# Performance work log

Hardware: AMD Instinct MI355X
Metric: run time of the kernel (lower is better)

Reference implementation:

```python
import jax, jax.numpy as jnp
import numpy as np

B, T, C = 2, 4096, 512
H, DH = 8, 64            # num_heads, num_head_channels (per-head dim after reshape)
COND = 512
SCALE = (DH // H) ** -0.5  # faithful to original: (num_head_channels // num_heads)**-0.5


def setup_inputs() -> dict:
    key = jax.random.key(0)
    ks = jax.random.split(key, 6)
    x = jax.random.normal(ks[0], (B, T, C), dtype=jnp.float32)
    condition = jax.random.normal(ks[1], (B, T, COND), dtype=jnp.float32)
    W_qk = jax.random.normal(ks[2], (COND, 2 * H * DH), dtype=jnp.float32) * (COND ** -0.5)
    W_v = jax.random.normal(ks[3], (C, H * DH), dtype=jnp.float32) * (C ** -0.5)
    W_u = jax.random.normal(ks[4], (H * DH, C), dtype=jnp.float32) * ((H * DH) ** -0.5)
    b_u = jax.random.normal(ks[5], (C,), dtype=jnp.float32) * 0.01
    return {"x": x, "condition": condition, "W_qk": W_qk, "W_v": W_v, "W_u": W_u, "b_u": b_u}


def reference(x, condition, W_qk, W_v, W_u, b_u):
    b, t, _ = x.shape
    qk = condition @ W_qk                                  # [b, t, 2*H*DH]
    q, k = jnp.split(qk, 2, axis=-1)
    q = q.reshape(b, t, H, DH).transpose(0, 2, 1, 3)       # [b, H, t, DH]
    k = k.reshape(b, t, H, DH).transpose(0, 2, 1, 3)
    v = (x @ W_v).reshape(b, t, H, DH).transpose(0, 2, 1, 3)
    q = q * SCALE
    dots = jnp.einsum('bhid,bhjd->bhij', q, k)             # [b, H, t, t] (1 GB score matrix)
    attn = jax.nn.softmax(dots, axis=-1)
    out = jnp.einsum('bhij,bhjd->bhid', attn, v)           # [b, H, t, DH]
    out = out.transpose(0, 2, 1, 3).reshape(b, t, H * DH)
    return out @ W_u + b_u
```

## Files before the change

kernel.cpp:

```cpp
#include <hip/hip_runtime.h>

#define B_SZ 2
#define T_SZ 4096

typedef unsigned short u16;
typedef __attribute__((ext_vector_type(8))) short short8;
typedef __attribute__((ext_vector_type(4))) float f32x4;
typedef __attribute__((ext_vector_type(4))) unsigned short u16x4;

#define CEXP 0.51006973f

__device__ __forceinline__ u16 f2bf(float f) {
    unsigned int u;
    __builtin_memcpy(&u, &f, 4);
    u = (u + 0x7fffu + ((u >> 16) & 1u)) >> 16;
    return (u16)u;
}
__device__ __forceinline__ unsigned int rbits(float f) {
    unsigned int u;
    __builtin_memcpy(&u, &f, 4);
    return u + 0x8000u;
}
__device__ __forceinline__ f32x4 mfma16(short8 a, short8 b, f32x4 c) {
    return __builtin_amdgcn_mfma_f32_16x16x32_bf16(a, b, c, 0, 0, 0);
}

__global__ void k_prep(const float* __restrict__ Wqk, const float* __restrict__ Wv,
                       const float* __restrict__ Wu, u16* __restrict__ Wqk_t,
                       u16* __restrict__ Wv_t, u16* __restrict__ Wu_t) {
    int blk = blockIdx.x, tid = threadIdx.x;
    __shared__ u16 T[64][72];
    const float* src; u16* dst; int N, ti;
    if (blk < 128)      { src = Wqk; dst = Wqk_t; N = 1024; ti = blk; }
    else if (blk < 192) { src = Wv;  dst = Wv_t;  N = 512;  ti = blk - 128; }
    else                { src = Wu;  dst = Wu_t;  N = 512;  ti = blk - 192; }
    int nt = N >> 6;
    int bi = ti / nt, bj = ti - bi * nt;
    int kb = bi * 64, nb = bj * 64;
    int r = tid >> 2, c4 = (tid & 3) * 16;
#pragma unroll
    for (int jj = 0; jj < 4; ++jj) {
        float4 v = *(const float4*)(src + (size_t)(kb + r) * N + nb + c4 + jj * 4);
        u16x4 w = { f2bf(v.x), f2bf(v.y), f2bf(v.z), f2bf(v.w) };
        *(u16x4*)(&T[r][c4 + jj * 4]) = w;
    }
    __syncthreads();
#pragma unroll
    for (int jj = 0; jj < 4; ++jj) {
        int c = c4 + jj * 4;
        u16x4 w = { T[c][r], T[c + 1][r], T[c + 2][r], T[c + 3][r] };
        *(u16x4*)(dst + (size_t)(nb + r) * 512 + kb + c) = w;
    }
}

template <typename OutT, int MODE, bool AF32, bool BF32, int TM, int TN>
__device__ __forceinline__ void gemm_body(int m0, int n0,
                                          const void* __restrict__ Ap, const void* __restrict__ Bp,
                                          const float* __restrict__ bias, OutT* __restrict__ C,
                                          OutT* __restrict__ C2, u16* As, u16* Bs) {
    const int K = 512;
    constexpr int BK = 64;
    constexpr int MI = TM / 32, NJ = TN / 32;
    constexpr int NAF = TM / 16, NAB = TM / 32;
    constexpr int NBF = TN / 16, NBB = TN / 32;
    int tid = threadIdx.x;
    int wave = tid >> 6, lane = tid & 63, l16 = lane & 15, q = lane >> 4;
    int mo = (wave & 1) * (TM / 2), no = (wave >> 1) * (TN / 2);

    f32x4 acc[MI][NJ];
#pragma unroll
    for (int i = 0; i < MI; ++i)
#pragma unroll
        for (int j = 0; j < NJ; ++j) acc[i][j] = (f32x4){0.f, 0.f, 0.f, 0.f};

    const float* Af = (const float*)Ap; const u16* Ab = (const u16*)Ap;
    const float* Bf = (const float*)Bp; const u16* Bb = (const u16*)Bp;

    const float* apf[NAF > 0 ? NAF : 1]; const u16* apb[NAB > 0 ? NAB : 1];
    const float* bpf[NBF > 0 ? NBF : 1]; const u16* bpb[NBB > 0 ? NBB : 1];
    float4 raf[NAF > 0 ? NAF : 1], rbf[NBF > 0 ? NBF : 1];
    short8 rab[NAB > 0 ? NAB : 1], rbb[NBB > 0 ? NBB : 1];

    if constexpr (AF32) {
#pragma unroll
        for (int jj = 0; jj < NAF; ++jj) {
            int id = tid + 256 * jj;
            apf[jj] = Af + (size_t)(m0 + (id >> 4)) * K + (id & 15) * 4;
            raf[jj] = *(const float4*)(apf[jj]);
        }
    } else {
#pragma unroll
        for (int jj = 0; jj < NAB; ++jj) {
            int id = tid + 256 * jj;
            apb[jj] = Ab + (size_t)(m0 + (id >> 3)) * K + (id & 7) * 8;
            rab[jj] = *(const short8*)(apb[jj]);
        }
    }
    if constexpr (BF32) {
#pragma unroll
        for (int jj = 0; jj < NBF; ++jj) {
            int id = tid + 256 * jj;
            bpf[jj] = Bf + (size_t)(n0 + (id >> 4)) * K + (id & 15) * 4;
            rbf[jj] = *(const float4*)(bpf[jj]);
        }
    } else {
#pragma unroll
        for (int jj = 0; jj < NBB; ++jj) {
            int id = tid + 256 * jj;
            bpb[jj] = Bb + (size_t)(n0 + (id >> 3)) * K + (id & 7) * 8;
            rbb[jj] = *(const short8*)(bpb[jj]);
        }
    }

#pragma unroll 1
    for (int k0 = 0; k0 < K; k0 += BK) {
        __syncthreads();
        if constexpr (AF32) {
#pragma unroll
            for (int jj = 0; jj < NAF; ++jj) {
                int id = tid + 256 * jj;
                u16x4 w = { f2bf(raf[jj].x), f2bf(raf[jj].y), f2bf(raf[jj].z), f2bf(raf[jj].w) };
                *(u16x4*)(&As[(id >> 4) * 72 + (id & 15) * 4]) = w;
            }
        } else {
#pragma unroll
            for (int jj = 0; jj < NAB; ++jj) {
                int id = tid + 256 * jj;
                *(short8*)(&As[(id >> 3) * 72 + (id & 7) * 8]) = rab[jj];
            }
        }
        if constexpr (BF32) {
#pragma unroll
            for (int jj = 0; jj < NBF; ++jj) {
                int id = tid + 256 * jj;
                u16x4 w = { f2bf(rbf[jj].x), f2bf(rbf[jj].y), f2bf(rbf[jj].z), f2bf(rbf[jj].w) };
                *(u16x4*)(&Bs[(id >> 4) * 72 + (id & 15) * 4]) = w;
            }
        } else {
#pragma unroll
            for (int jj = 0; jj < NBB; ++jj) {
                int id = tid + 256 * jj;
                *(short8*)(&Bs[(id >> 3) * 72 + (id & 7) * 8]) = rbb[jj];
            }
        }
        __syncthreads();

        int kadv = (k0 + BK < K) ? BK : 0;
        if constexpr (AF32) {
#pragma unroll
            for (int jj = 0; jj < NAF; ++jj) { apf[jj] += kadv; raf[jj] = *(const float4*)(apf[jj]); }
        } else {
#pragma unroll
            for (int jj = 0; jj < NAB; ++jj) { apb[jj] += kadv; rab[jj] = *(const short8*)(apb[jj]); }
        }
        if constexpr (BF32) {
#pragma unroll
            for (int jj = 0; jj < NBF; ++jj) { bpf[jj] += kadv; rbf[jj] = *(const float4*)(bpf[jj]); }
        } else {
#pragma unroll
            for (int jj = 0; jj < NBB; ++jj) { bpb[jj] += kadv; rbb[jj] = *(const short8*)(bpb[jj]); }
        }
        __builtin_amdgcn_sched_barrier(0);

#pragma unroll
        for (int kk = 0; kk < 2; ++kk) {
            short8 af[MI], bf[NJ];
#pragma unroll
            for (int i = 0; i < MI; ++i)
                af[i] = *(const short8*)(&As[(mo + i * 16 + l16) * 72 + kk * 32 + q * 8]);
#pragma unroll
            for (int j = 0; j < NJ; ++j)
                bf[j] = *(const short8*)(&Bs[(no + j * 16 + l16) * 72 + kk * 32 + q * 8]);
#pragma unroll
            for (int i = 0; i < MI; ++i)
#pragma unroll
                for (int j = 0; j < NJ; ++j) acc[i][j] = mfma16(af[i], bf[j], acc[i][j]);
        }
    }

#pragma unroll
    for (int i = 0; i < MI; ++i) {
        int mb = m0 + mo + i * 16 + q * 4;
#pragma unroll
        for (int j = 0; j < NJ; ++j) {
            int nc = n0 + no + j * 16 + l16;
            if constexpr (MODE == 0) {
                float4 bb = *(const float4*)(bias + mb);
                float4 w = { acc[i][j][0] + bb.x, acc[i][j][1] + bb.y,
                             acc[i][j][2] + bb.z, acc[i][j][3] + bb.w };
                *(float4*)(&C[(size_t)nc * 512 + mb]) = w;
            } else if constexpr (MODE == 1) {
                int b = nc >> 12, t = nc & 4095;
                int h = (mb & 511) >> 6, d = mb & 63;
                size_t addr = ((size_t)((b * 8 + h) * 4096 + t)) * 64 + d;
                if (mb < 512) {
                    u16x4 w = { f2bf(acc[i][j][0] * CEXP), f2bf(acc[i][j][1] * CEXP),
                                f2bf(acc[i][j][2] * CEXP), f2bf(acc[i][j][3] * CEXP) };
                    *(u16x4*)(&C[addr]) = w;
                } else {
                    u16x4 w = { f2bf(acc[i][j][0]), f2bf(acc[i][j][1]),
                                f2bf(acc[i][j][2]), f2bf(acc[i][j][3]) };
                    *(u16x4*)(&C2[addr]) = w;
                }
            } else {
                int b = mb >> 12, t = mb & 4095;
                int kt = t >> 6, k64 = t & 63;
                int h = nc >> 6, d = nc & 63;
                size_t addr = ((((size_t)(b * 8 + h) * 64 + kt) * 64 + d) << 6) + k64;
                u16x4 w = { f2bf(acc[i][j][0]), f2bf(acc[i][j][1]),
                            f2bf(acc[i][j][2]), f2bf(acc[i][j][3]) };
                *(u16x4*)(&C[addr]) = w;
            }
        }
    }
}

__global__ __launch_bounds__(256) void k_qkv(const u16* __restrict__ Wqk_t, const float* __restrict__ cond,
                                             const float* __restrict__ x, const u16* __restrict__ Wv_t,
                                             u16* __restrict__ Qh, u16* __restrict__ Kh,
                                             u16* __restrict__ Vb) {
    __shared__ __align__(16) u16 smem[(128 + 128) * 72];
    u16* As = smem;
    u16* Bs = smem + 128 * 72;
    int bid = blockIdx.x;
    if (bid < 512) {
        int bx = bid >> 6, by = bid & 63;
        gemm_body<u16, 1, false, true, 128, 128>(bx * 128, by * 128, Wqk_t, cond, nullptr, Qh, Kh, As, Bs);
    } else {
        int bid2 = bid - 512;
        int by = bid2 >> 6, bx = bid2 & 63;
        gemm_body<u16, 2, true, false, 128, 128>(bx * 128, by * 128, x, Wv_t, nullptr, Vb, nullptr, As, Bs);
    }
}

__global__ __launch_bounds__(256) void k_out(const u16* __restrict__ Wu_t, const u16* __restrict__ at,
                                             const float* __restrict__ bu, float* __restrict__ out) {
    __shared__ __align__(16) u16 smem[(128 + 128) * 72];
    int bid = blockIdx.x;
    int bx = bid >> 6, by = bid & 63;
    gemm_body<float, 0, false, false, 128, 128>(bx * 128, by * 128, Wu_t, at, bu, out, nullptr,
                                                smem, smem + 128 * 72);
}

__global__ __launch_bounds__(512) void k_flash(const u16* __restrict__ Qh, const u16* __restrict__ Kh,
                                               const u16* __restrict__ Vb, u16* __restrict__ o) {
    int bid = blockIdx.x;
    int h = bid & 7, qt = (bid >> 3) & 31, b = bid >> 8;
    int tid = threadIdx.x;
    int wave = tid >> 6, lane = tid & 63, l16 = lane & 15, q = lane >> 4;
    int ks = wave >> 2, w4 = wave & 3;
    int t256 = tid & 255;

    __shared__ __align__(16) u16 smem[2 * (64 * 80 + 64 * 72)];
    u16* Kt = smem + ks * (64 * 80 + 64 * 72);
    u16* Vt = Kt + 64 * 80;

    int head = b * 8 + h;
    short8 qf[2][2];
#pragma unroll
    for (int g = 0; g < 2; ++g) {
        const u16* qp = Qh + ((size_t)head * 4096 + qt * 128 + g * 64 + w4 * 16 + l16) * 64 + q * 8;
        qf[g][0] = *(const short8*)(qp);
        qf[g][1] = *(const short8*)(qp + 32);
    }

    const u16* kb = Kh + (size_t)head * 4096 * 64;
    const u16* vb = Vb + (size_t)head * 4096 * 64;

    int r0 = t256 >> 3, g0 = t256 & 7;
    u16* kw0 = &Kt[r0 * 80 + g0 * 8];
    u16* kw1 = &Kt[(r0 + 32) * 80 + g0 * 8];
    u16* vw0 = &Vt[r0 * 72 + g0 * 8];
    u16* vw1 = &Vt[(r0 + 32) * 72 + g0 * 8];

    f32x4 oacc[2][4];
#pragma unroll
    for (int g = 0; g < 2; ++g)
#pragma unroll
        for (int c = 0; c < 4; ++c) oacc[g][c] = (f32x4){0.f, 0.f, 0.f, 0.f};
    f32x4 lacc[2];
    lacc[0] = (f32x4){0.f, 0.f, 0.f, 0.f};
    lacc[1] = (f32x4){0.f, 0.f, 0.f, 0.f};
    const short8 ones = { 0x3F80, 0x3F80, 0x3F80, 0x3F80, 0x3F80, 0x3F80, 0x3F80, 0x3F80 };
    int pi0 = (l16 >> 2) * 8 + (l16 & 3);

    size_t off0 = (size_t)(ks * 32 + (qt & 31)) * 4096;
    short8 rk0 = *(const short8*)(kb + off0 + t256 * 8);
    short8 rk1 = *(const short8*)(kb + off0 + t256 * 8 + 2048);
    short8 rv0 = *(const short8*)(vb + off0 + t256 * 8);
    short8 rv1 = *(const short8*)(vb + off0 + t256 * 8 + 2048);

#pragma unroll 1
    for (int it = 0; it < 32; ++it) {
        __syncthreads();
        *(short8*)kw0 = rk0;
        *(short8*)kw1 = rk1;
        *(short8*)vw0 = rv0;
        *(short8*)vw1 = rv1;
        __syncthreads();

        size_t offn = (size_t)(ks * 32 + ((qt + it + 1) & 31)) * 4096;
        rk0 = *(const short8*)(kb + offn + t256 * 8);
        rk1 = *(const short8*)(kb + offn + t256 * 8 + 2048);
        rv0 = *(const short8*)(vb + offn + t256 * 8);
        rv1 = *(const short8*)(vb + offn + t256 * 8 + 2048);
        __builtin_amdgcn_sched_barrier(0);

#pragma unroll
        for (int kk = 0; kk < 2; ++kk) {
            const u16* ka = &Kt[(kk * 32 + pi0) * 80 + q * 8];
            short8 A00 = *(const short8*)(ka);
            short8 A01 = *(const short8*)(ka + 32);
            short8 A10 = *(const short8*)(ka + 4 * 80);
            short8 A11 = *(const short8*)(ka + 4 * 80 + 32);
            short8 vfc[4];
#pragma unroll
            for (int c = 0; c < 4; ++c)
                vfc[c] = *(const short8*)(&Vt[(c * 16 + l16) * 72 + kk * 32 + q * 8]);

#pragma unroll
            for (int g = 0; g < 2; ++g) {
                f32x4 s0 = (f32x4){0.f, 0.f, 0.f, 0.f};
                f32x4 s1 = (f32x4){0.f, 0.f, 0.f, 0.f};
                s0 = mfma16(A00, qf[g][0], s0); s0 = mfma16(A01, qf[g][1], s0);
                s1 = mfma16(A10, qf[g][0], s1); s1 = mfma16(A11, qf[g][1], s1);

                uint4 pd;
                pd.x = __builtin_amdgcn_perm(rbits(__builtin_amdgcn_exp2f(s0[1])),
                                             rbits(__builtin_amdgcn_exp2f(s0[0])), 0x07060302u);
                pd.y = __builtin_amdgcn_perm(rbits(__builtin_amdgcn_exp2f(s0[3])),
                                             rbits(__builtin_amdgcn_exp2f(s0[2])), 0x07060302u);
                pd.z = __builtin_amdgcn_perm(rbits(__builtin_amdgcn_exp2f(s1[1])),
                                             rbits(__builtin_amdgcn_exp2f(s1[0])), 0x07060302u);
                pd.w = __builtin_amdgcn_perm(rbits(__builtin_amdgcn_exp2f(s1[3])),
                                             rbits(__builtin_amdgcn_exp2f(s1[2])), 0x07060302u);
                short8 pf;
                __builtin_memcpy(&pf, &pd, 16);

                lacc[g] = mfma16(ones, pf, lacc[g]);
#pragma unroll
                for (int c = 0; c < 4; ++c)
                    oacc[g][c] = mfma16(vfc[c], pf, oacc[g][c]);
            }
        }
    }

    __syncthreads();
    float* red = (float*)smem;
    if (ks == 1) {
        float* rp = red + ((w4 * 64 + lane) * 37);
#pragma unroll
        for (int g = 0; g < 2; ++g)
#pragma unroll
            for (int c = 0; c < 4; ++c)
#pragma unroll
                for (int r = 0; r < 4; ++r) rp[g * 16 + c * 4 + r] = oacc[g][c][r];
        rp[32] = lacc[0][0];
        rp[33] = lacc[1][0];
    }
    __syncthreads();
    if (ks == 0) {
        const float* rp = red + ((w4 * 64 + lane) * 37);
#pragma unroll
        for (int g = 0; g < 2; ++g) {
#pragma unroll
            for (int c = 0; c < 4; ++c)
#pragma unroll
                for (int r = 0; r < 4; ++r) oacc[g][c][r] += rp[g * 16 + c * 4 + r];
            float inv = 1.f / (lacc[g][0] + rp[32 + g]);
            u16* ob = o + (size_t)(b * T_SZ + qt * 128 + g * 64 + w4 * 16 + l16) * 512 + h * 64 + q * 4;
#pragma unroll
            for (int c = 0; c < 4; ++c) {
                u16x4 w = { f2bf(oacc[g][c][0] * inv), f2bf(oacc[g][c][1] * inv),
                            f2bf(oacc[g][c][2] * inv), f2bf(oacc[g][c][3] * inv) };
                *(u16x4*)(ob + c * 16) = w;
            }
        }
    }
}

extern "C" void kernel_launch(void* const* d_in, const int* in_sizes, int n_in,
                              void* d_out, int out_size, void* d_ws, size_t ws_size,
                              hipStream_t stream) {
    const float* x    = (const float*)d_in[0];
    const float* cond = (const float*)d_in[1];
    const float* Wqk  = (const float*)d_in[2];
    const float* Wv   = (const float*)d_in[3];
    const float* Wu   = (const float*)d_in[4];
    const float* bu   = (const float*)d_in[5];
    float* out = (float*)d_out;

    const size_t MT = (size_t)B_SZ * T_SZ;
    u16* qh_ws = (u16*)d_ws;
    u16* kh_ws = qh_ws + MT * 512;
    u16* vb_ws = kh_ws + MT * 512;
    u16* at_ws = vb_ws + MT * 512;
    u16* Wqk_t = at_ws + MT * 512;
    u16* Wv_t  = Wqk_t + (size_t)1024 * 512;
    u16* Wu_t  = Wv_t + (size_t)512 * 512;

    k_prep<<<256, 256, 0, stream>>>(Wqk, Wv, Wu, Wqk_t, Wv_t, Wu_t);
    k_qkv<<<768, 256, 0, stream>>>(Wqk_t, cond, x, Wv_t, qh_ws, kh_ws, vb_ws);
    k_flash<<<512, 512, 0, stream>>>(qh_ws, kh_ws, vb_ws, at_ws);
    k_out<<<256, 256, 0, stream>>>(Wu_t, at_ws, bu, out);
}
```

Baseline: 203.3 us.

## Double-buffer flash K/V tiles and use direct global-to-LDS loads for bf16 GEMM weights

```diff
diff --git a/kernel.cpp b/kernel.cpp
--- a/kernel.cpp
+++ b/kernel.cpp
@@ -23,6 +23,10 @@
 }
 __device__ __forceinline__ f32x4 mfma16(short8 a, short8 b, f32x4 c) {
     return __builtin_amdgcn_mfma_f32_16x16x32_bf16(a, b, c, 0, 0, 0);
+}
+__device__ __forceinline__ void glds16(const u16* g, u16* l) {
+    __builtin_amdgcn_global_load_lds((const __attribute__((address_space(1))) void*)g,
+                                     (__attribute__((address_space(3))) void*)l, 16, 0, 0);
 }
 
 __global__ void k_prep(const float* __restrict__ Wqk, const float* __restrict__ Wv,
@@ -49,11 +53,14 @@
     for (int jj = 0; jj < 4; ++jj) {
         int c = c4 + jj * 4;
         u16x4 w = { T[c][r], T[c + 1][r], T[c + 2][r], T[c + 3][r] };
-        *(u16x4*)(dst + (size_t)(nb + r) * 512 + kb + c) = w;
-    }
-}
-
-template <typename OutT, int MODE, bool AF32, bool BF32, int TM, int TN>
+        int csw = (c & 7) | ((((c >> 3) ^ (r & 7))) << 3);
+        *(u16x4*)(dst + (size_t)(nb + r) * 512 + kb + csw) = w;
+    }
+}
+
+enum { ST_GLDS = 0, ST_F32 = 1, ST_BF16 = 2 };
+
+template <typename OutT, int MODE, int SA, int SB, int TM, int TN>
 __device__ __forceinline__ void gemm_body(int m0, int n0,
                                           const void* __restrict__ Ap, const void* __restrict__ Bp,
                                           const float* __restrict__ bias, OutT* __restrict__ C,
@@ -61,8 +68,8 @@
     const int K = 512;
     constexpr int BK = 64;
     constexpr int MI = TM / 32, NJ = TN / 32;
-    constexpr int NAF = TM / 16, NAB = TM / 32;
-    constexpr int NBF = TN / 16, NBB = TN / 32;
+    constexpr int NAF = TM / 16, NAB = TM / 32, NAG = TM / 32;
+    constexpr int NBF = TN / 16, NBB = TN / 32, NBG = TN / 32;
     int tid = threadIdx.x;
     int wave = tid >> 6, lane = tid & 63, l16 = lane & 15, q = lane >> 4;
     int mo = (wave & 1) * (TM / 2), no = (wave >> 1) * (TN / 2);
@@ -81,14 +88,14 @@
     float4 raf[NAF > 0 ? NAF : 1], rbf[NBF > 0 ? NBF : 1];
     short8 rab[NAB > 0 ? NAB : 1], rbb[NBB > 0 ? NBB : 1];
 
-    if constexpr (AF32) {
+    if constexpr (SA == ST_F32) {
 #pragma unroll
         for (int jj = 0; jj < NAF; ++jj) {
             int id = tid + 256 * jj;
             apf[jj] = Af + (size_t)(m0 + (id >> 4)) * K + (id & 15) * 4;
             raf[jj] = *(const float4*)(apf[jj]);
         }
-    } else {
+    } else if constexpr (SA == ST_BF16) {
 #pragma unroll
         for (int jj = 0; jj < NAB; ++jj) {
             int id = tid + 256 * jj;
@@ -96,14 +103,14 @@
             rab[jj] = *(const short8*)(apb[jj]);
         }
     }
-    if constexpr (BF32) {
+    if constexpr (SB == ST_F32) {
 #pragma unroll
         for (int jj = 0; jj < NBF; ++jj) {
             int id = tid + 256 * jj;
             bpf[jj] = Bf + (size_t)(n0 + (id >> 4)) * K + (id & 15) * 4;
             rbf[jj] = *(const float4*)(bpf[jj]);
         }
-    } else {
+    } else if constexpr (SB == ST_BF16) {
 #pragma unroll
         for (int jj = 0; jj < NBB; ++jj) {
             int id = tid + 256 * jj;
@@ -115,48 +122,64 @@
 #pragma unroll 1
     for (int k0 = 0; k0 < K; k0 += BK) {
         __syncthreads();
-        if constexpr (AF32) {
+        if constexpr (SA == ST_F32) {
 #pragma unroll
             for (int jj = 0; jj < NAF; ++jj) {
                 int id = tid + 256 * jj;
                 u16x4 w = { f2bf(raf[jj].x), f2bf(raf[jj].y), f2bf(raf[jj].z), f2bf(raf[jj].w) };
                 *(u16x4*)(&As[(id >> 4) * 72 + (id & 15) * 4]) = w;
             }
-        } else {
+        } else if constexpr (SA == ST_BF16) {
 #pragma unroll
             for (int jj = 0; jj < NAB; ++jj) {
                 int id = tid + 256 * jj;
                 *(short8*)(&As[(id >> 3) * 72 + (id & 7) * 8]) = rab[jj];
             }
         }
-        if constexpr (BF32) {
+        if constexpr (SB == ST_F32) {
 #pragma unroll
             for (int jj = 0; jj < NBF; ++jj) {
                 int id = tid + 256 * jj;
                 u16x4 w = { f2bf(rbf[jj].x), f2bf(rbf[jj].y), f2bf(rbf[jj].z), f2bf(rbf[jj].w) };
                 *(u16x4*)(&Bs[(id >> 4) * 72 + (id & 15) * 4]) = w;
             }
-        } else {
+        } else if constexpr (SB == ST_BF16) {
 #pragma unroll
             for (int jj = 0; jj < NBB; ++jj) {
                 int id = tid + 256 * jj;
                 *(short8*)(&Bs[(id >> 3) * 72 + (id & 7) * 8]) = rbb[jj];
             }
         }
+        if constexpr (SA == ST_GLDS) {
+            const u16* gbase = Ab + (size_t)m0 * K + k0;
+#pragma unroll
+            for (int jj = 0; jj < NAG; ++jj) {
+                int e = jj * 2048 + tid * 8;
+                glds16(gbase + (size_t)(e >> 6) * K + (e & 63), &As[e]);
+            }
+        }
+        if constexpr (SB == ST_GLDS) {
+            const u16* gbase = Bb + (size_t)n0 * K + k0;
+#pragma unroll
+            for (int jj = 0; jj < NBG; ++jj) {
+                int e = jj * 2048 + tid * 8;
+                glds16(gbase + (size_t)(e >> 6) * K + (e & 63), &Bs[e]);
+            }
+        }
         __syncthreads();
 
         int kadv = (k0 + BK < K) ? BK : 0;
-        if constexpr (AF32) {
+        if constexpr (SA == ST_F32) {
 #pragma unroll
             for (int jj = 0; jj < NAF; ++jj) { apf[jj] += kadv; raf[jj] = *(const float4*)(apf[jj]); }
-        } else {
+        } else if constexpr (SA == ST_BF16) {
 #pragma unroll
             for (int jj = 0; jj < NAB; ++jj) { apb[jj] += kadv; rab[jj] = *(const short8*)(apb[jj]); }
         }
-        if constexpr (BF32) {
+        if constexpr (SB == ST_F32) {
 #pragma unroll
             for (int jj = 0; jj < NBF; ++jj) { bpf[jj] += kadv; rbf[jj] = *(const float4*)(bpf[jj]); }
-        } else {
+        } else if constexpr (SB == ST_BF16) {
 #pragma unroll
             for (int jj = 0; jj < NBB; ++jj) { bpb[jj] += kadv; rbb[jj] = *(const short8*)(bpb[jj]); }
         }
@@ -166,11 +189,21 @@
         for (int kk = 0; kk < 2; ++kk) {
             short8 af[MI], bf[NJ];
 #pragma unroll
-            for (int i = 0; i < MI; ++i)
-                af[i] = *(const short8*)(&As[(mo + i * 16 + l16) * 72 + kk * 32 + q * 8]);
-#pragma unroll
-            for (int j = 0; j < NJ; ++j)
-                bf[j] = *(const short8*)(&Bs[(no + j * 16 + l16) * 72 + kk * 32 + q * 8]);
+            for (int i = 0; i < MI; ++i) {
+                int r = mo + i * 16 + l16;
+                if constexpr (SA == ST_GLDS)
+                    af[i] = *(const short8*)(&As[r * 64 + (((kk * 4 + q) ^ (l16 & 7)) << 3)]);
+                else
+                    af[i] = *(const short8*)(&As[r * 72 + kk * 32 + q * 8]);
+            }
+#pragma unroll
+            for (int j = 0; j < NJ; ++j) {
+                int r = no + j * 16 + l16;
+                if constexpr (SB == ST_GLDS)
+                    bf[j] = *(const short8*)(&Bs[r * 64 + (((kk * 4 + q) ^ (l16 & 7)) << 3)]);
+                else
+                    bf[j] = *(const short8*)(&Bs[r * 72 + kk * 32 + q * 8]);
+            }
 #pragma unroll
             for (int i = 0; i < MI; ++i)
 #pragma unroll
@@ -219,27 +252,27 @@
                                              const float* __restrict__ x, const u16* __restrict__ Wv_t,
                                              u16* __restrict__ Qh, u16* __restrict__ Kh,
                                              u16* __restrict__ Vb) {
-    __shared__ __align__(16) u16 smem[(128 + 128) * 72];
-    u16* As = smem;
-    u16* Bs = smem + 128 * 72;
+    __shared__ __align__(16) u16 smem[128 * 64 + 128 * 72];
     int bid = blockIdx.x;
     if (bid < 512) {
         int bx = bid >> 6, by = bid & 63;
-        gemm_body<u16, 1, false, true, 128, 128>(bx * 128, by * 128, Wqk_t, cond, nullptr, Qh, Kh, As, Bs);
+        gemm_body<u16, 1, ST_GLDS, ST_F32, 128, 128>(bx * 128, by * 128, Wqk_t, cond, nullptr,
+                                                     Qh, Kh, smem, smem + 128 * 64);
     } else {
         int bid2 = bid - 512;
         int by = bid2 >> 6, bx = bid2 & 63;
-        gemm_body<u16, 2, true, false, 128, 128>(bx * 128, by * 128, x, Wv_t, nullptr, Vb, nullptr, As, Bs);
+        gemm_body<u16, 2, ST_F32, ST_GLDS, 128, 128>(bx * 128, by * 128, x, Wv_t, nullptr,
+                                                     Vb, nullptr, smem, smem + 128 * 72);
     }
 }
 
 __global__ __launch_bounds__(256) void k_out(const u16* __restrict__ Wu_t, const u16* __restrict__ at,
                                              const float* __restrict__ bu, float* __restrict__ out) {
-    __shared__ __align__(16) u16 smem[(128 + 128) * 72];
+    __shared__ __align__(16) u16 smem[128 * 64 + 128 * 72];
     int bid = blockIdx.x;
     int bx = bid >> 6, by = bid & 63;
-    gemm_body<float, 0, false, false, 128, 128>(bx * 128, by * 128, Wu_t, at, bu, out, nullptr,
-                                                smem, smem + 128 * 72);
+    gemm_body<float, 0, ST_GLDS, ST_BF16, 128, 128>(bx * 128, by * 128, Wu_t, at, bu, out, nullptr,
+                                                    smem, smem + 128 * 64);
 }
 
 __global__ __launch_bounds__(512) void k_flash(const u16* __restrict__ Qh, const u16* __restrict__ Kh,
@@ -251,9 +284,10 @@
     int ks = wave >> 2, w4 = wave & 3;
     int t256 = tid & 255;
 
-    __shared__ __align__(16) u16 smem[2 * (64 * 80 + 64 * 72)];
-    u16* Kt = smem + ks * (64 * 80 + 64 * 72);
-    u16* Vt = Kt + 64 * 80;
+    const int TSZ = 64 * 80 + 64 * 72;
+    __shared__ __align__(16) u16 smem[2 * 2 * (64 * 80 + 64 * 72)];
+    u16* Kt0 = smem + ks * 2 * TSZ;
+    u16* Vt0 = Kt0 + 64 * 80;
 
     int head = b * 8 + h;
     short8 qf[2][2];
@@ -268,10 +302,10 @@
     const u16* vb = Vb + (size_t)head * 4096 * 64;
 
     int r0 = t256 >> 3, g0 = t256 & 7;
-    u16* kw0 = &Kt[r0 * 80 + g0 * 8];
-    u16* kw1 = &Kt[(r0 + 32) * 80 + g0 * 8];
-    u16* vw0 = &Vt[r0 * 72 + g0 * 8];
-    u16* vw1 = &Vt[(r0 + 32) * 72 + g0 * 8];
+    u16* kw0 = &Kt0[r0 * 80 + g0 * 8];
+    u16* kw1 = &Kt0[(r0 + 32) * 80 + g0 * 8];
+    u16* vw0 = &Vt0[r0 * 72 + g0 * 8];
+    u16* vw1 = &Vt0[(r0 + 32) * 72 + g0 * 8];
 
     f32x4 oacc[2][4];
 #pragma unroll
@@ -284,31 +318,43 @@
     const short8 ones = { 0x3F80, 0x3F80, 0x3F80, 0x3F80, 0x3F80, 0x3F80, 0x3F80, 0x3F80 };
     int pi0 = (l16 >> 2) * 8 + (l16 & 3);
 
-    size_t off0 = (size_t)(ks * 32 + (qt & 31)) * 4096;
-    short8 rk0 = *(const short8*)(kb + off0 + t256 * 8);
-    short8 rk1 = *(const short8*)(kb + off0 + t256 * 8 + 2048);
-    short8 rv0 = *(const short8*)(vb + off0 + t256 * 8);
-    short8 rv1 = *(const short8*)(vb + off0 + t256 * 8 + 2048);
+    size_t offA = (size_t)(ks * 32 + (qt & 31)) * 4096;
+    short8 rk0 = *(const short8*)(kb + offA + t256 * 8);
+    short8 rk1 = *(const short8*)(kb + offA + t256 * 8 + 2048);
+    short8 rv0 = *(const short8*)(vb + offA + t256 * 8);
+    short8 rv1 = *(const short8*)(vb + offA + t256 * 8 + 2048);
+    *(short8*)kw0 = rk0;
+    *(short8*)kw1 = rk1;
+    *(short8*)vw0 = rv0;
+    *(short8*)vw1 = rv1;
+    size_t offB = (size_t)(ks * 32 + ((qt + 1) & 31)) * 4096;
+    rk0 = *(const short8*)(kb + offB + t256 * 8);
+    rk1 = *(const short8*)(kb + offB + t256 * 8 + 2048);
+    rv0 = *(const short8*)(vb + offB + t256 * 8);
+    rv1 = *(const short8*)(vb + offB + t256 * 8 + 2048);
 
 #pragma unroll 1
     for (int it = 0; it < 32; ++it) {
         __syncthreads();
-        *(short8*)kw0 = rk0;
-        *(short8*)kw1 = rk1;
-        *(short8*)vw0 = rv0;
-        *(short8*)vw1 = rv1;
-        __syncthreads();
-
-        size_t offn = (size_t)(ks * 32 + ((qt + it + 1) & 31)) * 4096;
+        int wb = (it + 1) & 1;
+        *(short8*)(kw0 + wb * TSZ) = rk0;
+        *(short8*)(kw1 + wb * TSZ) = rk1;
+        *(short8*)(vw0 + wb * TSZ) = rv0;
+        *(short8*)(vw1 + wb * TSZ) = rv1;
+
+        size_t offn = (size_t)(ks * 32 + ((qt + it + 2) & 31)) * 4096;
         rk0 = *(const short8*)(kb + offn + t256 * 8);
         rk1 = *(const short8*)(kb + offn + t256 * 8 + 2048);
         rv0 = *(const short8*)(vb + offn + t256 * 8);
         rv1 = *(const short8*)(vb + offn + t256 * 8 + 2048);
         __builtin_amdgcn_sched_barrier(0);
 
+        const u16* Ktc = Kt0 + (it & 1) * TSZ;
+        const u16* Vtc = Ktc + 64 * 80;
+
 #pragma unroll
         for (int kk = 0; kk < 2; ++kk) {
-            const u16* ka = &Kt[(kk * 32 + pi0) * 80 + q * 8];
+            const u16* ka = &Ktc[(kk * 32 + pi0) * 80 + q * 8];
             short8 A00 = *(const short8*)(ka);
             short8 A01 = *(const short8*)(ka + 32);
             short8 A10 = *(const short8*)(ka + 4 * 80);
@@ -316,7 +362,7 @@
             short8 vfc[4];
 #pragma unroll
             for (int c = 0; c < 4; ++c)
-                vfc[c] = *(const short8*)(&Vt[(c * 16 + l16) * 72 + kk * 32 + q * 8]);
+                vfc[c] = *(const short8*)(&Vtc[(c * 16 + l16) * 72 + kk * 32 + q * 8]);
 
 #pragma unroll
             for (int g = 0; g < 2; ++g) {
```

Result: slower. 208.0 us (+2.3%).

## Use direct global-to-LDS loads with XOR-swizzled bf16 layouts in projection GEMMs

Applied to the files above, without the earlier changes.

```diff
diff --git a/kernel.cpp b/kernel.cpp
--- a/kernel.cpp
+++ b/kernel.cpp
@@ -24,45 +24,70 @@
 __device__ __forceinline__ f32x4 mfma16(short8 a, short8 b, f32x4 c) {
     return __builtin_amdgcn_mfma_f32_16x16x32_bf16(a, b, c, 0, 0, 0);
 }
+__device__ __forceinline__ void glds16(const u16* g, u16* l) {
+    __builtin_amdgcn_global_load_lds((const __attribute__((address_space(1))) void*)g,
+                                     (__attribute__((address_space(3))) void*)l, 16, 0, 0);
+}
+
 
 __global__ void k_prep(const float* __restrict__ Wqk, const float* __restrict__ Wv,
-                       const float* __restrict__ Wu, u16* __restrict__ Wqk_t,
-                       u16* __restrict__ Wv_t, u16* __restrict__ Wu_t) {
+                       const float* __restrict__ Wu, const float* __restrict__ cond,
+                       const float* __restrict__ x, u16* __restrict__ Wqk_t,
+                       u16* __restrict__ Wv_t, u16* __restrict__ Wu_t,
+                       u16* __restrict__ cond_bf, u16* __restrict__ x_bf) {
     int blk = blockIdx.x, tid = threadIdx.x;
     __shared__ u16 T[64][72];
-    const float* src; u16* dst; int N, ti;
-    if (blk < 128)      { src = Wqk; dst = Wqk_t; N = 1024; ti = blk; }
-    else if (blk < 192) { src = Wv;  dst = Wv_t;  N = 512;  ti = blk - 128; }
-    else                { src = Wu;  dst = Wu_t;  N = 512;  ti = blk - 192; }
-    int nt = N >> 6;
-    int bi = ti / nt, bj = ti - bi * nt;
-    int kb = bi * 64, nb = bj * 64;
-    int r = tid >> 2, c4 = (tid & 3) * 16;
-#pragma unroll
-    for (int jj = 0; jj < 4; ++jj) {
-        float4 v = *(const float4*)(src + (size_t)(kb + r) * N + nb + c4 + jj * 4);
-        u16x4 w = { f2bf(v.x), f2bf(v.y), f2bf(v.z), f2bf(v.w) };
-        *(u16x4*)(&T[r][c4 + jj * 4]) = w;
-    }
-    __syncthreads();
-#pragma unroll
-    for (int jj = 0; jj < 4; ++jj) {
-        int c = c4 + jj * 4;
-        u16x4 w = { T[c][r], T[c + 1][r], T[c + 2][r], T[c + 3][r] };
-        *(u16x4*)(dst + (size_t)(nb + r) * 512 + kb + c) = w;
-    }
-}
-
-template <typename OutT, int MODE, bool AF32, bool BF32, int TM, int TN>
-__device__ __forceinline__ void gemm_body(int m0, int n0,
-                                          const void* __restrict__ Ap, const void* __restrict__ Bp,
+    if (blk < 256) {
+        const float* src; u16* dst; int N, ti;
+        if (blk < 128)      { src = Wqk; dst = Wqk_t; N = 1024; ti = blk; }
+        else if (blk < 192) { src = Wv;  dst = Wv_t;  N = 512;  ti = blk - 128; }
+        else                { src = Wu;  dst = Wu_t;  N = 512;  ti = blk - 192; }
+        int nt = N >> 6;
+        int bi = ti / nt, bj = ti - bi * nt;
+        int kb = bi * 64, nb = bj * 64;
+        int r = tid >> 2, c4 = (tid & 3) * 16;
+#pragma unroll
+        for (int jj = 0; jj < 4; ++jj) {
+            float4 v = *(const float4*)(src + (size_t)(kb + r) * N + nb + c4 + jj * 4);
+            u16x4 w = { f2bf(v.x), f2bf(v.y), f2bf(v.z), f2bf(v.w) };
+            *(u16x4*)(&T[r][c4 + jj * 4]) = w;
+        }
+        __syncthreads();
+#pragma unroll
+        for (int jj = 0; jj < 4; ++jj) {
+            int c = c4 + jj * 4;
+            u16x4 w = { T[c][r], T[c + 1][r], T[c + 2][r], T[c + 3][r] };
+            int csw = (c & 7) | ((((c >> 3) ^ (r & 7))) << 3);
+            *(u16x4*)(dst + (size_t)(nb + r) * 512 + kb + csw) = w;
+        }
+    } else {
+        int t = (blk - 256) * 256 + tid;
+#pragma unroll
+        for (int it = 0; it < 4; ++it, t += 262144) {
+            int sel = t >> 19;
+            const float* s = sel ? x : cond;
+            u16* d = sel ? x_bf : cond_bf;
+            int g = t & 524287;
+            int row = g >> 6, g6 = g & 63;
+            float4 a = *(const float4*)(s + (size_t)g * 8);
+            float4 b = *(const float4*)(s + (size_t)g * 8 + 4);
+            short8 w = { (short)f2bf(a.x), (short)f2bf(a.y), (short)f2bf(a.z), (short)f2bf(a.w),
+                         (short)f2bf(b.x), (short)f2bf(b.y), (short)f2bf(b.z), (short)f2bf(b.w) };
+            int off = row * 512 + ((g6 >> 3) << 6) + (((g6 & 7) ^ (row & 7)) << 3);
+            *(short8*)(d + off) = w;
+        }
+    }
+}
+
+template <typename OutT, int MODE, int TM, int TN>
+__device__ __forceinline__ void gemm_glds(int m0, int n0,
+                                          const u16* __restrict__ A, const u16* __restrict__ B,
                                           const float* __restrict__ bias, OutT* __restrict__ C,
                                           OutT* __restrict__ C2, u16* As, u16* Bs) {
     const int K = 512;
     constexpr int BK = 64;
     constexpr int MI = TM / 32, NJ = TN / 32;
-    constexpr int NAF = TM / 16, NAB = TM / 32;
-    constexpr int NBF = TN / 16, NBB = TN / 32;
+    constexpr int NAG = TM / 32, NBG = TN / 32;
     int tid = threadIdx.x;
     int wave = tid >> 6, lane = tid & 63, l16 = lane & 15, q = lane >> 4;
     int mo = (wave & 1) * (TM / 2), no = (wave >> 1) * (TN / 2);
@@ -73,104 +98,38 @@
 #pragma unroll
         for (int j = 0; j < NJ; ++j) acc[i][j] = (f32x4){0.f, 0.f, 0.f, 0.f};
 
-    const float* Af = (const float*)Ap; const u16* Ab = (const u16*)Ap;
-    const float* Bf = (const float*)Bp; const u16* Bb = (const u16*)Bp;
-
-    const float* apf[NAF > 0 ? NAF : 1]; const u16* apb[NAB > 0 ? NAB : 1];
-    const float* bpf[NBF > 0 ? NBF : 1]; const u16* bpb[NBB > 0 ? NBB : 1];
-    float4 raf[NAF > 0 ? NAF : 1], rbf[NBF > 0 ? NBF : 1];
-    short8 rab[NAB > 0 ? NAB : 1], rbb[NBB > 0 ? NBB : 1];
-
-    if constexpr (AF32) {
-#pragma unroll
-        for (int jj = 0; jj < NAF; ++jj) {
-            int id = tid + 256 * jj;
-            apf[jj] = Af + (size_t)(m0 + (id >> 4)) * K + (id & 15) * 4;
-            raf[jj] = *(const float4*)(apf[jj]);
-        }
-    } else {
-#pragma unroll
-        for (int jj = 0; jj < NAB; ++jj) {
-            int id = tid + 256 * jj;
-            apb[jj] = Ab + (size_t)(m0 + (id >> 3)) * K + (id & 7) * 8;
-            rab[jj] = *(const short8*)(apb[jj]);
-        }
-    }
-    if constexpr (BF32) {
-#pragma unroll
-        for (int jj = 0; jj < NBF; ++jj) {
-            int id = tid + 256 * jj;
-            bpf[jj] = Bf + (size_t)(n0 + (id >> 4)) * K + (id & 15) * 4;
-            rbf[jj] = *(const float4*)(bpf[jj]);
-        }
-    } else {
-#pragma unroll
-        for (int jj = 0; jj < NBB; ++jj) {
-            int id = tid + 256 * jj;
-            bpb[jj] = Bb + (size_t)(n0 + (id >> 3)) * K + (id & 7) * 8;
-            rbb[jj] = *(const short8*)(bpb[jj]);
-        }
-    }
-
 #pragma unroll 1
     for (int k0 = 0; k0 < K; k0 += BK) {
         __syncthreads();
-        if constexpr (AF32) {
-#pragma unroll
-            for (int jj = 0; jj < NAF; ++jj) {
-                int id = tid + 256 * jj;
-                u16x4 w = { f2bf(raf[jj].x), f2bf(raf[jj].y), f2bf(raf[jj].z), f2bf(raf[jj].w) };
-                *(u16x4*)(&As[(id >> 4) * 72 + (id & 15) * 4]) = w;
-            }
-        } else {
-#pragma unroll
-            for (int jj = 0; jj < NAB; ++jj) {
-                int id = tid + 256 * jj;
-                *(short8*)(&As[(id >> 3) * 72 + (id & 7) * 8]) = rab[jj];
-            }
-        }
-        if constexpr (BF32) {
-#pragma unroll
-            for (int jj = 0; jj < NBF; ++jj) {
-                int id = tid + 256 * jj;
-                u16x4 w = { f2bf(rbf[jj].x), f2bf(rbf[jj].y), f2bf(rbf[jj].z), f2bf(rbf[jj].w) };
-                *(u16x4*)(&Bs[(id >> 4) * 72 + (id & 15) * 4]) = w;
-            }
-        } else {
-#pragma unroll
-            for (int jj = 0; jj < NBB; ++jj) {
-                int id = tid + 256 * jj;
-                *(short8*)(&Bs[(id >> 3) * 72 + (id & 7) * 8]) = rbb[jj];
-            }
-        }
-        __syncthreads();
-
-        int kadv = (k0 + BK < K) ? BK : 0;
-        if constexpr (AF32) {
-#pragma unroll
-            for (int jj = 0; jj < NAF; ++jj) { apf[jj] += kadv; raf[jj] = *(const float4*)(apf[jj]); }
-        } else {
-#pragma unroll
-            for (int jj = 0; jj < NAB; ++jj) { apb[jj] += kadv; rab[jj] = *(const short8*)(apb[jj]); }
-        }
-        if constexpr (BF32) {
-#pragma unroll
-            for (int jj = 0; jj < NBF; ++jj) { bpf[jj] += kadv; rbf[jj] = *(const float4*)(bpf[jj]); }
-        } else {
-#pragma unroll
-            for (int jj = 0; jj < NBB; ++jj) { bpb[jj] += kadv; rbb[jj] = *(const short8*)(bpb[jj]); }
-        }
-        __builtin_amdgcn_sched_barrier(0);
+        {
+            const u16* ga = A + (size_t)m0 * K + k0;
+#pragma unroll
+            for (int jj = 0; jj < NAG; ++jj) {
+                int e = jj * 2048 + tid * 8;
+                glds16(ga + (size_t)(e >> 6) * K + (e & 63), &As[e]);
+            }
+            const u16* gb = B + (size_t)n0 * K + k0;
+#pragma unroll
+            for (int jj = 0; jj < NBG; ++jj) {
+                int e = jj * 2048 + tid * 8;
+                glds16(gb + (size_t)(e >> 6) * K + (e & 63), &Bs[e]);
+            }
+        }
+        __syncthreads();
 
 #pragma unroll
         for (int kk = 0; kk < 2; ++kk) {
             short8 af[MI], bf[NJ];
 #pragma unroll
-            for (int i = 0; i < MI; ++i)
-                af[i] = *(const short8*)(&As[(mo + i * 16 + l16) * 72 + kk * 32 + q * 8]);
-#pragma unroll
-            for (int j = 0; j < NJ; ++j)
-                bf[j] = *(const short8*)(&Bs[(no + j * 16 + l16) * 72 + kk * 32 + q * 8]);
+            for (int i = 0; i < MI; ++i) {
+                int r = mo + i * 16 + l16;
+                af[i] = *(const short8*)(&As[r * 64 + (((kk * 4 + q) ^ (l16 & 7)) << 3)]);
+            }
+#pragma unroll
+            for (int j = 0; j < NJ; ++j) {
+                int r = no + j * 16 + l16;
+                bf[j] = *(const short8*)(&Bs[r * 64 + (((kk * 4 + q) ^ (l16 & 7)) << 3)]);
+            }
 #pragma unroll
             for (int i = 0; i < MI; ++i)
 #pragma unroll
@@ -215,31 +174,31 @@
     }
 }
 
-__global__ __launch_bounds__(256) void k_qkv(const u16* __restrict__ Wqk_t, const float* __restrict__ cond,
-                                             const float* __restrict__ x, const u16* __restrict__ Wv_t,
+__global__ __launch_bounds__(256) void k_qkv(const u16* __restrict__ Wqk_t, const u16* __restrict__ cond_bf,
+                                             const u16* __restrict__ x_bf, const u16* __restrict__ Wv_t,
                                              u16* __restrict__ Qh, u16* __restrict__ Kh,
                                              u16* __restrict__ Vb) {
-    __shared__ __align__(16) u16 smem[(128 + 128) * 72];
-    u16* As = smem;
-    u16* Bs = smem + 128 * 72;
+    __shared__ __align__(16) u16 smem[2 * 128 * 64];
     int bid = blockIdx.x;
     if (bid < 512) {
         int bx = bid >> 6, by = bid & 63;
-        gemm_body<u16, 1, false, true, 128, 128>(bx * 128, by * 128, Wqk_t, cond, nullptr, Qh, Kh, As, Bs);
+        gemm_glds<u16, 1, 128, 128>(bx * 128, by * 128, Wqk_t, cond_bf, nullptr,
+                                    Qh, Kh, smem, smem + 128 * 64);
     } else {
         int bid2 = bid - 512;
         int by = bid2 >> 6, bx = bid2 & 63;
-        gemm_body<u16, 2, true, false, 128, 128>(bx * 128, by * 128, x, Wv_t, nullptr, Vb, nullptr, As, Bs);
+        gemm_glds<u16, 2, 128, 128>(bx * 128, by * 128, x_bf, Wv_t, nullptr,
+                                    Vb, nullptr, smem, smem + 128 * 64);
     }
 }
 
 __global__ __launch_bounds__(256) void k_out(const u16* __restrict__ Wu_t, const u16* __restrict__ at,
                                              const float* __restrict__ bu, float* __restrict__ out) {
-    __shared__ __align__(16) u16 smem[(128 + 128) * 72];
+    __shared__ __align__(16) u16 smem[2 * 128 * 64];
     int bid = blockIdx.x;
     int bx = bid >> 6, by = bid & 63;
-    gemm_body<float, 0, false, false, 128, 128>(bx * 128, by * 128, Wu_t, at, bu, out, nullptr,
-                                                smem, smem + 128 * 72);
+    gemm_glds<float, 0, 128, 128>(bx * 128, by * 128, Wu_t, at, bu, out, nullptr,
+                                  smem, smem + 128 * 64);
 }
 
 __global__ __launch_bounds__(512) void k_flash(const u16* __restrict__ Qh, const u16* __restrict__ Kh,
@@ -361,6 +320,7 @@
     __syncthreads();
     if (ks == 0) {
         const float* rp = red + ((w4 * 64 + lane) * 37);
+        int xg = l16 & 7;
 #pragma unroll
         for (int g = 0; g < 2; ++g) {
 #pragma unroll
@@ -368,12 +328,13 @@
 #pragma unroll
                 for (int r = 0; r < 4; ++r) oacc[g][c][r] += rp[g * 16 + c * 4 + r];
             float inv = 1.f / (lacc[g][0] + rp[32 + g]);
-            u16* ob = o + (size_t)(b * T_SZ + qt * 128 + g * 64 + w4 * 16 + l16) * 512 + h * 64 + q * 4;
+            u16* ob = o + (size_t)(b * T_SZ + qt * 128 + g * 64 + w4 * 16 + l16) * 512
+                        + h * 64 + (q & 1) * 4;
 #pragma unroll
             for (int c = 0; c < 4; ++c) {
                 u16x4 w = { f2bf(oacc[g][c][0] * inv), f2bf(oacc[g][c][1] * inv),
                             f2bf(oacc[g][c][2] * inv), f2bf(oacc[g][c][3] * inv) };
-                *(u16x4*)(ob + c * 16) = w;
+                *(u16x4*)(ob + (((c * 2 + (q >> 1)) ^ xg) << 3)) = w;
             }
         }
     }
@@ -398,9 +359,11 @@
     u16* Wqk_t = at_ws + MT * 512;
     u16* Wv_t  = Wqk_t + (size_t)1024 * 512;
     u16* Wu_t  = Wv_t + (size_t)512 * 512;
-
-    k_prep<<<256, 256, 0, stream>>>(Wqk, Wv, Wu, Wqk_t, Wv_t, Wu_t);
-    k_qkv<<<768, 256, 0, stream>>>(Wqk_t, cond, x, Wv_t, qh_ws, kh_ws, vb_ws);
+    u16* xb_ws = Wu_t + (size_t)512 * 512;
+    u16* cb_ws = at_ws;
+
+    k_prep<<<1280, 256, 0, stream>>>(Wqk, Wv, Wu, cond, x, Wqk_t, Wv_t, Wu_t, cb_ws, xb_ws);
+    k_qkv<<<768, 256, 0, stream>>>(Wqk_t, cb_ws, xb_ws, Wv_t, qh_ws, kh_ws, vb_ws);
     k_flash<<<512, 512, 0, stream>>>(qh_ws, kh_ws, vb_ws, at_ws);
     k_out<<<256, 256, 0, stream>>>(Wu_t, at_ws, bu, out);
 }
```

Result: slower. 208.7 us (+2.6%).
